# Kernel tuning notes

Measured on AMD Instinct MI355X. Metric: run time of the kernel, lower is better.

The kernel has to match this reference:

```python
import jax, jax.numpy as jnp
import numpy as np

B, N, K, C, CE, H = 2, 2048, 48, 128, 128, 128
IN = 2 * C + CE  # 384
AGG_SCALE = 30.0
LN_EPS = 1e-5


def setup_inputs() -> dict:
    key = jax.random.key(0)
    ks = jax.random.split(key, 12)
    inp = {
        "node_h": jax.random.normal(ks[0], (B, N, C), jnp.float32),
        "edge_h": jax.random.normal(ks[1], (B, N, K, CE), jnp.float32),
        "edge_index": jax.random.randint(ks[2], (B, N, K), 0, N, jnp.int64),
        # message MLP: Linear(IN,H) GELU Linear(H,H) GELU Linear(H,C)
        "W1": jax.random.normal(ks[3], (IN, H), jnp.float32) / np.sqrt(IN),
        "b1": jnp.zeros((H,), jnp.float32),
        "W2": jax.random.normal(ks[4], (H, H), jnp.float32) / np.sqrt(H),
        "b2": jnp.zeros((H,), jnp.float32),
        "W3": jax.random.normal(ks[5], (H, C), jnp.float32) / np.sqrt(H),
        "b3": jnp.zeros((C,), jnp.float32),
        "Wu": jax.random.normal(ks[6], (C, C), jnp.float32) / np.sqrt(C),
        "bu": jnp.zeros((C,), jnp.float32),
        "ln_g": jnp.ones((C,), jnp.float32),
        "ln_b": jnp.zeros((C,), jnp.float32),
    }
    return inp


def _layer_norm(x, g, b):
    mu = jnp.mean(x, axis=-1, keepdims=True)
    var = jnp.var(x, axis=-1, keepdims=True)
    return (x - mu) * jax.lax.rsqrt(var + LN_EPS) * g + b


def _gelu(x):
    return jax.nn.gelu(x, approximate=False)  # torch nn.GELU default (erf)


def reference(node_h, edge_h, edge_index, W1, b1, W2, b2, W3, b3, Wu, bu, ln_g, ln_b):
    b, n, k = edge_index.shape
    c = node_h.shape[-1]
    # gather neighbor node features: (B,N,K,C)
    node_j = jnp.take_along_axis(
        node_h, edge_index.reshape(b, n * k)[..., None], axis=1
    ).reshape(b, n, k, c)
    node_i = jnp.broadcast_to(node_h[:, :, None, :], (b, n, k, c))
    edge_packed = jnp.concatenate([node_i, node_j, edge_h], axis=-1)  # (B,N,K,IN)
    # message MLP
    h = _gelu(edge_packed @ W1 + b1)
    h = _gelu(h @ W2 + b2)
    messages = (h @ W3 + b3).sum(axis=-2) / AGG_SCALE  # (B,N,C)
    # dropout is identity in eval mode
    updated_nodes = _layer_norm(node_h + messages, ln_g, ln_b)
    node_updates = updated_nodes @ Wu + bu
    out = _layer_norm(node_h + node_updates, ln_g, ln_b)
    return out
```

## Files before the change

### kernel.cpp

```cpp
#include <hip/hip_runtime.h>
#include <hip/hip_bf16.h>
#include <math.h>

#define Bn   2
#define Nn   2048
#define Kn   48
#define Cn   128
#define G2   16

typedef short bf16x8 __attribute__((ext_vector_type(8)));
typedef float f32x4  __attribute__((ext_vector_type(4)));

#if __has_builtin(__builtin_amdgcn_cvt_pk_bf16_f32)
#define HAS_PK 1
#endif

__device__ __forceinline__ short f2bf(float f) {
  union { float f; unsigned u; } v; v.f = f;
  unsigned r = v.u + 0x7fffu + ((v.u >> 16) & 1u);
  return (short)(r >> 16);
}

__device__ __forceinline__ unsigned pk2(float a, float b) {
#ifdef HAS_PK
  auto p = __builtin_amdgcn_cvt_pk_bf16_f32(a, b);
  return __builtin_bit_cast(unsigned, p);
#else
  return (unsigned)(unsigned short)f2bf(a) | ((unsigned)(unsigned short)f2bf(b) << 16);
#endif
}

__device__ __forceinline__ float gelu_f(float x) {
  float z = x * (-2.3021991f - 0.10294200f * x * x);
  float e = __builtin_amdgcn_exp2f(z);
  return x * __builtin_amdgcn_rcpf(1.0f + e);
}

__global__ void pack_weights(const float* __restrict__ W1,
                             const float* __restrict__ W2,
                             const float* __restrict__ W3,
                             const float* __restrict__ Wu,
                             short* __restrict__ ws) {
  int tid = blockIdx.x * blockDim.x + threadIdx.x;
  if (tid >= 192 * 64) return;
  int lane = tid & 63;
  int tile = tid >> 6;
  const float* W; short* dst;
  if (tile < 32)       { W = W1;         dst = ws; }
  else if (tile < 96)  { W = W1 + 16384; dst = ws + 16384; tile -= 32; }
  else if (tile < 128) { W = W2;         dst = ws + 49152; tile -= 96; }
  else if (tile < 160) { W = W3;         dst = ws + 65536; tile -= 128; }
  else                 { W = Wu;         dst = ws + 81920; tile -= 160; }
  int kt = tile >> 3, nt = tile & 7;
  int n  = nt * 16 + (lane & 15);
  int k0 = kt * 32 + (lane >> 4) * 8;
  union { short s[8]; bf16x8 v; } u8;
#pragma unroll
  for (int j = 0; j < 8; j++) u8.s[j] = f2bf(W[(k0 + j) * 128 + n]);
  *reinterpret_cast<bf16x8*>(dst + (tile << 9) + lane * 8) = u8.v;
}

__global__ __launch_bounds__(256, 6)
void node_update_kernel(const float* __restrict__ node_h,
                        const float* __restrict__ edge_h,
                        const int*   __restrict__ edge_index,
                        const short* __restrict__ wpack,
                        const float* __restrict__ b1,
                        const float* __restrict__ b2,
                        float* __restrict__ hs_out) {
  __shared__ __align__(16) char smem[25024];
  short* Xs    = (short*)smem;
  short* H1s   = (short*)(smem + 12288);
  short* nhb   = (short*)(smem + 24576);
  int*   idx_s = (int*)  (smem + 24832);

  const int tid  = threadIdx.x;
  const int blk  = blockIdx.x;
  const int bb   = blk >> 11;
  const int lane = tid & 63;
  const int wave = tid >> 6;
  const int lr   = lane & 15;
  const int lq   = lane >> 4;

  const short* W1i = wpack;
  const short* W1e = wpack + 16384;
  const short* W2p = wpack + 49152;

  if (tid < 128) {
    nhb[tid] = f2bf(node_h[(size_t)blk * Cn + tid]);
  } else if (tid < 176) {
    idx_s[tid - 128] = edge_index[blk * Kn + (tid - 128)];
  }
  __syncthreads();

  {
    const int w  = tid & 31;
    const int rr = tid >> 5;
#pragma unroll
    for (int k = 0; k < 6; k++) {
      int r = rr + k * 8;
      const float* src = (w < 16)
          ? node_h + (size_t)(bb * Nn + idx_s[r]) * Cn + w * 8
          : edge_h + ((size_t)blk * Kn + r) * Cn + (w - 16) * 8;
      float4 v0 = *reinterpret_cast<const float4*>(src);
      float4 v1 = *reinterpret_cast<const float4*>(src + 4);
      uint4 p;
      p.x = pk2(v0.x, v0.y); p.y = pk2(v0.z, v0.w);
      p.z = pk2(v1.x, v1.y); p.w = pk2(v1.z, v1.w);
      *reinterpret_cast<uint4*>(&Xs[r * 256 + ((w ^ (r & 7)) << 3)]) = p;
    }
  }

  f32x4 accY[2] = {};
#pragma unroll
  for (int kt = 0; kt < 4; kt++) {
    bf16x8 av = {};
    if (lr == 0) av = *reinterpret_cast<const bf16x8*>(&nhb[kt * 32 + lq * 8]);
    bf16x8 bv0 = *reinterpret_cast<const bf16x8*>(W1i + ((kt * 8 + wave * 2 + 0) << 9) + lane * 8);
    bf16x8 bv1 = *reinterpret_cast<const bf16x8*>(W1i + ((kt * 8 + wave * 2 + 1) << 9) + lane * 8);
    accY[0] = __builtin_amdgcn_mfma_f32_16x16x32_bf16(av, bv0, accY[0], 0, 0, 0);
    accY[1] = __builtin_amdgcn_mfma_f32_16x16x32_bf16(av, bv1, accY[1], 0, 0, 0);
  }
  __syncthreads();

  f32x4 acc[3][2] = {};
#pragma unroll
  for (int kt = 0; kt < 8; kt++) {
    bf16x8 bf0 = *reinterpret_cast<const bf16x8*>(W1e + ((kt * 8 + wave * 2 + 0) << 9) + lane * 8);
    bf16x8 bf1 = *reinterpret_cast<const bf16x8*>(W1e + ((kt * 8 + wave * 2 + 1) << 9) + lane * 8);
    int sw = (((kt * 4 + lq) ^ (lr & 7)) << 3);
    bf16x8 a0 = *reinterpret_cast<const bf16x8*>(&Xs[(0  + lr) * 256 + sw]);
    bf16x8 a1 = *reinterpret_cast<const bf16x8*>(&Xs[(16 + lr) * 256 + sw]);
    bf16x8 a2 = *reinterpret_cast<const bf16x8*>(&Xs[(32 + lr) * 256 + sw]);
    acc[0][0] = __builtin_amdgcn_mfma_f32_16x16x32_bf16(a0, bf0, acc[0][0], 0, 0, 0);
    acc[0][1] = __builtin_amdgcn_mfma_f32_16x16x32_bf16(a0, bf1, acc[0][1], 0, 0, 0);
    acc[1][0] = __builtin_amdgcn_mfma_f32_16x16x32_bf16(a1, bf0, acc[1][0], 0, 0, 0);
    acc[1][1] = __builtin_amdgcn_mfma_f32_16x16x32_bf16(a1, bf1, acc[1][1], 0, 0, 0);
    acc[2][0] = __builtin_amdgcn_mfma_f32_16x16x32_bf16(a2, bf0, acc[2][0], 0, 0, 0);
    acc[2][1] = __builtin_amdgcn_mfma_f32_16x16x32_bf16(a2, bf1, acc[2][1], 0, 0, 0);
  }
  __syncthreads();

#pragma unroll
  for (int j = 0; j < 2; j++) {
    int col = (wave * 2 + j) * 16 + lr;
    float yi = __shfl(accY[j][0], lr) + b1[col];
    int g = col >> 3, cl = col & 7;
#pragma unroll
    for (int mt = 0; mt < 3; mt++) {
      int r0 = mt * 16 + lq * 4;
      float g0 = gelu_f(acc[mt][j][0] + yi);
      float g1 = gelu_f(acc[mt][j][1] + yi);
      float g2 = gelu_f(acc[mt][j][2] + yi);
      float g3 = gelu_f(acc[mt][j][3] + yi);
      unsigned p01 = pk2(g0, g1), p23 = pk2(g2, g3);
      H1s[(r0 + 0) * 128 + ((g ^ ((r0 + 0) & 7)) << 3) + cl] = (short)(p01 & 0xffff);
      H1s[(r0 + 1) * 128 + ((g ^ ((r0 + 1) & 7)) << 3) + cl] = (short)(p01 >> 16);
      H1s[(r0 + 2) * 128 + ((g ^ ((r0 + 2) & 7)) << 3) + cl] = (short)(p23 & 0xffff);
      H1s[(r0 + 3) * 128 + ((g ^ ((r0 + 3) & 7)) << 3) + cl] = (short)(p23 >> 16);
    }
  }
  __syncthreads();

  f32x4 acc2[3][2] = {};
#pragma unroll
  for (int kt = 0; kt < 4; kt++) {
    bf16x8 bf0 = *reinterpret_cast<const bf16x8*>(W2p + ((kt * 8 + wave * 2 + 0) << 9) + lane * 8);
    bf16x8 bf1 = *reinterpret_cast<const bf16x8*>(W2p + ((kt * 8 + wave * 2 + 1) << 9) + lane * 8);
    int sw = (((kt * 4 + lq) ^ (lr & 7)) << 3);
    bf16x8 a0 = *reinterpret_cast<const bf16x8*>(&H1s[(0  + lr) * 128 + sw]);
    bf16x8 a1 = *reinterpret_cast<const bf16x8*>(&H1s[(16 + lr) * 128 + sw]);
    bf16x8 a2 = *reinterpret_cast<const bf16x8*>(&H1s[(32 + lr) * 128 + sw]);
    acc2[0][0] = __builtin_amdgcn_mfma_f32_16x16x32_bf16(a0, bf0, acc2[0][0], 0, 0, 0);
    acc2[0][1] = __builtin_amdgcn_mfma_f32_16x16x32_bf16(a0, bf1, acc2[0][1], 0, 0, 0);
    acc2[1][0] = __builtin_amdgcn_mfma_f32_16x16x32_bf16(a1, bf0, acc2[1][0], 0, 0, 0);
    acc2[1][1] = __builtin_amdgcn_mfma_f32_16x16x32_bf16(a1, bf1, acc2[1][1], 0, 0, 0);
    acc2[2][0] = __builtin_amdgcn_mfma_f32_16x16x32_bf16(a2, bf0, acc2[2][0], 0, 0, 0);
    acc2[2][1] = __builtin_amdgcn_mfma_f32_16x16x32_bf16(a2, bf1, acc2[2][1], 0, 0, 0);
  }
#pragma unroll
  for (int j = 0; j < 2; j++) {
    int col = (wave * 2 + j) * 16 + lr;
    float bias = b2[col];
    float s = 0.f;
#pragma unroll
    for (int mt = 0; mt < 3; mt++)
#pragma unroll
      for (int r = 0; r < 4; r++) s += gelu_f(acc2[mt][j][r] + bias);
    s += __shfl_xor(s, 16);
    s += __shfl_xor(s, 32);
    if (lq == 0) hs_out[(size_t)blk * Cn + col] = s;
  }
}

__global__ __launch_bounds__(256, 4)
void tail_kernel(const float* __restrict__ node_h,
                 const short* __restrict__ wpack,
                 const float* __restrict__ b3,
                 const float* __restrict__ bu,
                 const float* __restrict__ ln_g,
                 const float* __restrict__ ln_b,
                 float* __restrict__ out) {
  __shared__ __align__(16) char sm2[24832];
  short* hsB = (short*)sm2;
  float* nhr = (float*)(sm2 + 4096);
  float* xs  = (float*)(sm2 + 12288);
  short* usB = (short*)(sm2 + 20736);

  const int tid  = threadIdx.x;
  const int lane = tid & 63;
  const int wave = tid >> 6;
  const int lr   = lane & 15;
  const int lq   = lane >> 4;
  const int n0   = blockIdx.x * G2;

  const short* W3p = wpack + 65536;
  const short* Wup = wpack + 81920;

  {
    int row = tid >> 4, seg = tid & 15;
    const float* p = node_h + (size_t)(n0 + row) * Cn + seg * 8;
    float4 a0 = *reinterpret_cast<const float4*>(p);
    float4 a1 = *reinterpret_cast<const float4*>(p + 4);
    *reinterpret_cast<float4*>(&nhr[row * 128 + seg * 8])     = a0;
    *reinterpret_cast<float4*>(&nhr[row * 128 + seg * 8 + 4]) = a1;
    const float* q = out + (size_t)(n0 + row) * Cn + seg * 8;
    float4 c0 = *reinterpret_cast<const float4*>(q);
    float4 c1 = *reinterpret_cast<const float4*>(q + 4);
    uint4 pk;
    pk.x = pk2(c0.x, c0.y); pk.y = pk2(c0.z, c0.w);
    pk.z = pk2(c1.x, c1.y); pk.w = pk2(c1.z, c1.w);
    *reinterpret_cast<uint4*>(&hsB[row * 128 + ((seg ^ (row & 7)) << 3)]) = pk;
  }
  __syncthreads();

  f32x4 am[2] = {};
#pragma unroll
  for (int kt = 0; kt < 4; kt++) {
    bf16x8 av = *reinterpret_cast<const bf16x8*>(&hsB[lr * 128 + (((kt * 4 + lq) ^ (lr & 7)) << 3)]);
    bf16x8 bv0 = *reinterpret_cast<const bf16x8*>(W3p + ((kt * 8 + wave * 2 + 0) << 9) + lane * 8);
    bf16x8 bv1 = *reinterpret_cast<const bf16x8*>(W3p + ((kt * 8 + wave * 2 + 1) << 9) + lane * 8);
    am[0] = __builtin_amdgcn_mfma_f32_16x16x32_bf16(av, bv0, am[0], 0, 0, 0);
    am[1] = __builtin_amdgcn_mfma_f32_16x16x32_bf16(av, bv1, am[1], 0, 0, 0);
  }
#pragma unroll
  for (int j = 0; j < 2; j++) {
    int col = (wave * 2 + j) * 16 + lr;
    float bb = 48.0f * b3[col];
#pragma unroll
    for (int r = 0; r < 4; r++) {
      int row = lq * 4 + r;
      xs[row * 132 + col] = nhr[row * 128 + col] + (am[j][r] + bb) * (1.0f / 30.0f);
    }
  }
  __syncthreads();

  const float lg1 = ln_g[lane],      lb1v = ln_b[lane];
  const float lg2 = ln_g[lane + 64], lb2v = ln_b[lane + 64];
#pragma unroll
  for (int s = 0; s < 4; s++) {
    int row = wave * 4 + s;
    float v1 = xs[row * 132 + lane];
    float v2 = xs[row * 132 + lane + 64];
    float s1 = v1 + v2, s2 = v1 * v1 + v2 * v2;
#pragma unroll
    for (int off = 32; off >= 1; off >>= 1) {
      s1 += __shfl_xor(s1, off);
      s2 += __shfl_xor(s2, off);
    }
    float mu = s1 * (1.f / 128.f);
    float var = s2 * (1.f / 128.f) - mu * mu;
    float rstd = rsqrtf(var + 1e-5f);
    unsigned u12 = pk2((v1 - mu) * rstd * lg1 + lb1v,
                       (v2 - mu) * rstd * lg2 + lb2v);
    int sw = (row & 7);
    usB[row * 128 + (((lane >> 3) ^ sw) << 3) + (lane & 7)]       = (short)(u12 & 0xffff);
    usB[row * 128 + ((((lane >> 3) + 8) ^ sw) << 3) + (lane & 7)] = (short)(u12 >> 16);
  }
  __syncthreads();

  f32x4 au[2] = {};
#pragma unroll
  for (int kt = 0; kt < 4; kt++) {
    bf16x8 av = *reinterpret_cast<const bf16x8*>(&usB[lr * 128 + (((kt * 4 + lq) ^ (lr & 7)) << 3)]);
    bf16x8 bv0 = *reinterpret_cast<const bf16x8*>(Wup + ((kt * 8 + wave * 2 + 0) << 9) + lane * 8);
    bf16x8 bv1 = *reinterpret_cast<const bf16x8*>(Wup + ((kt * 8 + wave * 2 + 1) << 9) + lane * 8);
    au[0] = __builtin_amdgcn_mfma_f32_16x16x32_bf16(av, bv0, au[0], 0, 0, 0);
    au[1] = __builtin_amdgcn_mfma_f32_16x16x32_bf16(av, bv1, au[1], 0, 0, 0);
  }
  __syncthreads();
#pragma unroll
  for (int j = 0; j < 2; j++) {
    int col = (wave * 2 + j) * 16 + lr;
    float bb = bu[col];
#pragma unroll
    for (int r = 0; r < 4; r++) {
      int row = lq * 4 + r;
      xs[row * 132 + col] = nhr[row * 128 + col] + au[j][r] + bb;
    }
  }
  __syncthreads();

#pragma unroll
  for (int s = 0; s < 4; s++) {
    int row = wave * 4 + s;
    float v1 = xs[row * 132 + lane];
    float v2 = xs[row * 132 + lane + 64];
    float s1 = v1 + v2, s2 = v1 * v1 + v2 * v2;
#pragma unroll
    for (int off = 32; off >= 1; off >>= 1) {
      s1 += __shfl_xor(s1, off);
      s2 += __shfl_xor(s2, off);
    }
    float mu = s1 * (1.f / 128.f);
    float var = s2 * (1.f / 128.f) - mu * mu;
    float rstd = rsqrtf(var + 1e-5f);
    out[(size_t)(n0 + row) * Cn + lane]      = (v1 - mu) * rstd * lg1 + lb1v;
    out[(size_t)(n0 + row) * Cn + lane + 64] = (v2 - mu) * rstd * lg2 + lb2v;
  }
}

extern "C" void kernel_launch(void* const* d_in, const int* in_sizes, int n_in,
                              void* d_out, int out_size, void* d_ws, size_t ws_size,
                              hipStream_t stream) {
  const float* node_h     = (const float*)d_in[0];
  const float* edge_h     = (const float*)d_in[1];
  const int*   edge_index = (const int*)  d_in[2];
  const float* W1 = (const float*)d_in[3];
  const float* b1 = (const float*)d_in[4];
  const float* W2 = (const float*)d_in[5];
  const float* b2 = (const float*)d_in[6];
  const float* W3 = (const float*)d_in[7];
  const float* b3 = (const float*)d_in[8];
  const float* Wu = (const float*)d_in[9];
  const float* bu = (const float*)d_in[10];
  const float* ln_g = (const float*)d_in[11];
  const float* ln_b = (const float*)d_in[12];
  float* out   = (float*)d_out;
  short* wpack = (short*)d_ws;

  pack_weights<<<48, 256, 0, stream>>>(W1, W2, W3, Wu, wpack);
  node_update_kernel<<<Bn * Nn, 256, 0, stream>>>(
      node_h, edge_h, edge_index, wpack, b1, b2, out);
  tail_kernel<<<(Bn * Nn) / G2, 256, 0, stream>>>(
      node_h, wpack, b3, bu, ln_g, ln_b, out);
}
```

Measured before the change: 204.5 us.

## Fuse tail W3/LayerNorm/Wu/LayerNorm stage into per-node message kernel

Removes the separate tail kernel and runs the W3 projection, both LayerNorms and the Wu projection at the end of the per-node kernel, one node per block. The aim is to drop a kernel launch and the global round-trip of the aggregated hidden sums. The cost is poor MFMA use: a single row is padded to 16 (only lr==0 lanes feed data), and the main kernel gains extra barriers and serial tail work per block.

```diff
diff --git a/kernel.cpp b/kernel.cpp
--- a/kernel.cpp
+++ b/kernel.cpp
@@ -6,7 +6,6 @@
 #define Nn   2048
 #define Kn   48
 #define Cn   128
-#define G2   16
 
 typedef short bf16x8 __attribute__((ext_vector_type(8)));
 typedef float f32x4  __attribute__((ext_vector_type(4)));
@@ -67,12 +66,19 @@
                         const short* __restrict__ wpack,
                         const float* __restrict__ b1,
                         const float* __restrict__ b2,
-                        float* __restrict__ hs_out) {
+                        const float* __restrict__ b3,
+                        const float* __restrict__ bu,
+                        const float* __restrict__ ln_g,
+                        const float* __restrict__ ln_b,
+                        float* __restrict__ out) {
   __shared__ __align__(16) char smem[25024];
   short* Xs    = (short*)smem;
   short* H1s   = (short*)(smem + 12288);
   short* nhb   = (short*)(smem + 24576);
   int*   idx_s = (int*)  (smem + 24832);
+  short* hsA   = (short*)smem;
+  float* xsA   = (float*)(smem + 512);
+  short* usA   = (short*)(smem + 1024);
 
   const int tid  = threadIdx.x;
   const int blk  = blockIdx.x;
@@ -85,6 +91,8 @@
   const short* W1i = wpack;
   const short* W1e = wpack + 16384;
   const short* W2p = wpack + 49152;
+  const short* W3p = wpack + 65536;
+  const short* Wup = wpack + 81920;
 
   if (tid < 128) {
     nhb[tid] = f2bf(node_h[(size_t)blk * Cn + tid]);
@@ -189,79 +197,32 @@
       for (int r = 0; r < 4; r++) s += gelu_f(acc2[mt][j][r] + bias);
     s += __shfl_xor(s, 16);
     s += __shfl_xor(s, 32);
-    if (lq == 0) hs_out[(size_t)blk * Cn + col] = s;
-  }
-}
-
-__global__ __launch_bounds__(256, 4)
-void tail_kernel(const float* __restrict__ node_h,
-                 const short* __restrict__ wpack,
-                 const float* __restrict__ b3,
-                 const float* __restrict__ bu,
-                 const float* __restrict__ ln_g,
-                 const float* __restrict__ ln_b,
-                 float* __restrict__ out) {
-  __shared__ __align__(16) char sm2[24832];
-  short* hsB = (short*)sm2;
-  float* nhr = (float*)(sm2 + 4096);
-  float* xs  = (float*)(sm2 + 12288);
-  short* usB = (short*)(sm2 + 20736);
-
-  const int tid  = threadIdx.x;
-  const int lane = tid & 63;
-  const int wave = tid >> 6;
-  const int lr   = lane & 15;
-  const int lq   = lane >> 4;
-  const int n0   = blockIdx.x * G2;
-
-  const short* W3p = wpack + 65536;
-  const short* Wup = wpack + 81920;
-
-  {
-    int row = tid >> 4, seg = tid & 15;
-    const float* p = node_h + (size_t)(n0 + row) * Cn + seg * 8;
-    float4 a0 = *reinterpret_cast<const float4*>(p);
-    float4 a1 = *reinterpret_cast<const float4*>(p + 4);
-    *reinterpret_cast<float4*>(&nhr[row * 128 + seg * 8])     = a0;
-    *reinterpret_cast<float4*>(&nhr[row * 128 + seg * 8 + 4]) = a1;
-    const float* q = out + (size_t)(n0 + row) * Cn + seg * 8;
-    float4 c0 = *reinterpret_cast<const float4*>(q);
-    float4 c1 = *reinterpret_cast<const float4*>(q + 4);
-    uint4 pk;
-    pk.x = pk2(c0.x, c0.y); pk.y = pk2(c0.z, c0.w);
-    pk.z = pk2(c1.x, c1.y); pk.w = pk2(c1.z, c1.w);
-    *reinterpret_cast<uint4*>(&hsB[row * 128 + ((seg ^ (row & 7)) << 3)]) = pk;
-  }
-  __syncthreads();
-
-  f32x4 am[2] = {};
-#pragma unroll
-  for (int kt = 0; kt < 4; kt++) {
-    bf16x8 av = *reinterpret_cast<const bf16x8*>(&hsB[lr * 128 + (((kt * 4 + lq) ^ (lr & 7)) << 3)]);
+    if (lq == 0) hsA[col] = f2bf(s);
+  }
+  __syncthreads();
+
+  f32x4 mv[2] = {};
+#pragma unroll
+  for (int kt = 0; kt < 4; kt++) {
+    bf16x8 av = {};
+    if (lr == 0) av = *reinterpret_cast<const bf16x8*>(&hsA[kt * 32 + lq * 8]);
     bf16x8 bv0 = *reinterpret_cast<const bf16x8*>(W3p + ((kt * 8 + wave * 2 + 0) << 9) + lane * 8);
     bf16x8 bv1 = *reinterpret_cast<const bf16x8*>(W3p + ((kt * 8 + wave * 2 + 1) << 9) + lane * 8);
-    am[0] = __builtin_amdgcn_mfma_f32_16x16x32_bf16(av, bv0, am[0], 0, 0, 0);
-    am[1] = __builtin_amdgcn_mfma_f32_16x16x32_bf16(av, bv1, am[1], 0, 0, 0);
-  }
-#pragma unroll
-  for (int j = 0; j < 2; j++) {
-    int col = (wave * 2 + j) * 16 + lr;
-    float bb = 48.0f * b3[col];
-#pragma unroll
-    for (int r = 0; r < 4; r++) {
-      int row = lq * 4 + r;
-      xs[row * 132 + col] = nhr[row * 128 + col] + (am[j][r] + bb) * (1.0f / 30.0f);
-    }
-  }
-  __syncthreads();
-
-  const float lg1 = ln_g[lane],      lb1v = ln_b[lane];
-  const float lg2 = ln_g[lane + 64], lb2v = ln_b[lane + 64];
-#pragma unroll
-  for (int s = 0; s < 4; s++) {
-    int row = wave * 4 + s;
-    float v1 = xs[row * 132 + lane];
-    float v2 = xs[row * 132 + lane + 64];
+    mv[0] = __builtin_amdgcn_mfma_f32_16x16x32_bf16(av, bv0, mv[0], 0, 0, 0);
+    mv[1] = __builtin_amdgcn_mfma_f32_16x16x32_bf16(av, bv1, mv[1], 0, 0, 0);
+  }
+  if (lq == 0) {
+#pragma unroll
+    for (int j = 0; j < 2; j++) {
+      int col = (wave * 2 + j) * 16 + lr;
+      xsA[col] = node_h[(size_t)blk * Cn + col]
+               + (mv[j][0] + 48.0f * b3[col]) * (1.0f / 30.0f);
+    }
+  }
+  __syncthreads();
+
+  if (wave == 0) {
+    float v1 = xsA[lane], v2 = xsA[lane + 64];
     float s1 = v1 + v2, s2 = v1 * v1 + v2 * v2;
 #pragma unroll
     for (int off = 32; off >= 1; off >>= 1) {
@@ -271,41 +232,34 @@
     float mu = s1 * (1.f / 128.f);
     float var = s2 * (1.f / 128.f) - mu * mu;
     float rstd = rsqrtf(var + 1e-5f);
-    unsigned u12 = pk2((v1 - mu) * rstd * lg1 + lb1v,
-                       (v2 - mu) * rstd * lg2 + lb2v);
-    int sw = (row & 7);
-    usB[row * 128 + (((lane >> 3) ^ sw) << 3) + (lane & 7)]       = (short)(u12 & 0xffff);
-    usB[row * 128 + ((((lane >> 3) + 8) ^ sw) << 3) + (lane & 7)] = (short)(u12 >> 16);
-  }
-  __syncthreads();
-
-  f32x4 au[2] = {};
-#pragma unroll
-  for (int kt = 0; kt < 4; kt++) {
-    bf16x8 av = *reinterpret_cast<const bf16x8*>(&usB[lr * 128 + (((kt * 4 + lq) ^ (lr & 7)) << 3)]);
+    unsigned u12 = pk2((v1 - mu) * rstd * ln_g[lane] + ln_b[lane],
+                       (v2 - mu) * rstd * ln_g[lane + 64] + ln_b[lane + 64]);
+    usA[lane]      = (short)(u12 & 0xffff);
+    usA[lane + 64] = (short)(u12 >> 16);
+  }
+  __syncthreads();
+
+  f32x4 uv[2] = {};
+#pragma unroll
+  for (int kt = 0; kt < 4; kt++) {
+    bf16x8 av = {};
+    if (lr == 0) av = *reinterpret_cast<const bf16x8*>(&usA[kt * 32 + lq * 8]);
     bf16x8 bv0 = *reinterpret_cast<const bf16x8*>(Wup + ((kt * 8 + wave * 2 + 0) << 9) + lane * 8);
     bf16x8 bv1 = *reinterpret_cast<const bf16x8*>(Wup + ((kt * 8 + wave * 2 + 1) << 9) + lane * 8);
-    au[0] = __builtin_amdgcn_mfma_f32_16x16x32_bf16(av, bv0, au[0], 0, 0, 0);
-    au[1] = __builtin_amdgcn_mfma_f32_16x16x32_bf16(av, bv1, au[1], 0, 0, 0);
-  }
-  __syncthreads();
-#pragma unroll
-  for (int j = 0; j < 2; j++) {
-    int col = (wave * 2 + j) * 16 + lr;
-    float bb = bu[col];
-#pragma unroll
-    for (int r = 0; r < 4; r++) {
-      int row = lq * 4 + r;
-      xs[row * 132 + col] = nhr[row * 128 + col] + au[j][r] + bb;
-    }
-  }
-  __syncthreads();
-
-#pragma unroll
-  for (int s = 0; s < 4; s++) {
-    int row = wave * 4 + s;
-    float v1 = xs[row * 132 + lane];
-    float v2 = xs[row * 132 + lane + 64];
+    uv[0] = __builtin_amdgcn_mfma_f32_16x16x32_bf16(av, bv0, uv[0], 0, 0, 0);
+    uv[1] = __builtin_amdgcn_mfma_f32_16x16x32_bf16(av, bv1, uv[1], 0, 0, 0);
+  }
+  if (lq == 0) {
+#pragma unroll
+    for (int j = 0; j < 2; j++) {
+      int col = (wave * 2 + j) * 16 + lr;
+      xsA[col] = node_h[(size_t)blk * Cn + col] + uv[j][0] + bu[col];
+    }
+  }
+  __syncthreads();
+
+  if (wave == 0) {
+    float v1 = xsA[lane], v2 = xsA[lane + 64];
     float s1 = v1 + v2, s2 = v1 * v1 + v2 * v2;
 #pragma unroll
     for (int off = 32; off >= 1; off >>= 1) {
@@ -315,8 +269,8 @@
     float mu = s1 * (1.f / 128.f);
     float var = s2 * (1.f / 128.f) - mu * mu;
     float rstd = rsqrtf(var + 1e-5f);
-    out[(size_t)(n0 + row) * Cn + lane]      = (v1 - mu) * rstd * lg1 + lb1v;
-    out[(size_t)(n0 + row) * Cn + lane + 64] = (v2 - mu) * rstd * lg2 + lb2v;
+    out[(size_t)blk * Cn + lane]      = (v1 - mu) * rstd * ln_g[lane] + ln_b[lane];
+    out[(size_t)blk * Cn + lane + 64] = (v2 - mu) * rstd * ln_g[lane + 64] + ln_b[lane + 64];
   }
 }
 
@@ -341,7 +295,5 @@
 
   pack_weights<<<48, 256, 0, stream>>>(W1, W2, W3, Wu, wpack);
   node_update_kernel<<<Bn * Nn, 256, 0, stream>>>(
-      node_h, edge_h, edge_index, wpack, b1, b2, out);
-  tail_kernel<<<(Bn * Nn) / G2, 256, 0, stream>>>(
-      node_h, wpack, b3, bu, ln_g, ln_b, out);
-}
+      node_h, edge_h, edge_index, wpack, b1, b2, b3, bu, ln_g, ln_b, out);
+}
```

New measurement: 220.1 us. +7.6%, slower.

## Process two nodes per block with eight waves each owning one output column tile

Applied to the files above, without the earlier changes.

The node update kernel now handles two nodes per 512-thread block, giving 96 edge rows per block. Each of the eight waves owns a single 16-column output tile and loops over six row tiles, so each wave loads half as many weight fragments per row. This is meant to cut the global weight fragment traffic per edge and halve the block count. The cost is doubled shared memory per block (about 50 KB) and a larger block size, which may limit how many blocks fit on a CU.

```diff
diff --git a/kernel.cpp b/kernel.cpp
--- a/kernel.cpp
+++ b/kernel.cpp
@@ -60,7 +60,7 @@
   *reinterpret_cast<bf16x8*>(dst + (tile << 9) + lane * 8) = u8.v;
 }
 
-__global__ __launch_bounds__(256, 6)
+__global__ __launch_bounds__(512, 6)
 void node_update_kernel(const float* __restrict__ node_h,
                         const float* __restrict__ edge_h,
                         const int*   __restrict__ edge_index,
@@ -68,15 +68,15 @@
                         const float* __restrict__ b1,
                         const float* __restrict__ b2,
                         float* __restrict__ hs_out) {
-  __shared__ __align__(16) char smem[25024];
+  __shared__ __align__(16) char smem[50048];
   short* Xs    = (short*)smem;
-  short* H1s   = (short*)(smem + 12288);
-  short* nhb   = (short*)(smem + 24576);
-  int*   idx_s = (int*)  (smem + 24832);
+  short* H1s   = (short*)(smem + 24576);
+  short* nhb   = (short*)(smem + 49152);
+  int*   idx_s = (int*)  (smem + 49664);
 
   const int tid  = threadIdx.x;
-  const int blk  = blockIdx.x;
-  const int bb   = blk >> 11;
+  const int n0   = blockIdx.x * 2;
+  const int bb   = n0 >> 11;
   const int lane = tid & 63;
   const int wave = tid >> 6;
   const int lr   = lane & 15;
@@ -86,10 +86,10 @@
   const short* W1e = wpack + 16384;
   const short* W2p = wpack + 49152;
 
-  if (tid < 128) {
-    nhb[tid] = f2bf(node_h[(size_t)blk * Cn + tid]);
-  } else if (tid < 176) {
-    idx_s[tid - 128] = edge_index[blk * Kn + (tid - 128)];
+  if (tid < 256) {
+    nhb[tid] = f2bf(node_h[(size_t)n0 * Cn + tid]);
+  } else if (tid < 352) {
+    idx_s[tid - 256] = edge_index[n0 * Kn + (tid - 256)];
   }
   __syncthreads();
 
@@ -98,10 +98,10 @@
     const int rr = tid >> 5;
 #pragma unroll
     for (int k = 0; k < 6; k++) {
-      int r = rr + k * 8;
+      int r = rr + k * 16;
       const float* src = (w < 16)
           ? node_h + (size_t)(bb * Nn + idx_s[r]) * Cn + w * 8
-          : edge_h + ((size_t)blk * Kn + r) * Cn + (w - 16) * 8;
+          : edge_h + ((size_t)n0 * Kn + r) * Cn + (w - 16) * 8;
       float4 v0 = *reinterpret_cast<const float4*>(src);
       float4 v1 = *reinterpret_cast<const float4*>(src + 4);
       uint4 p;
@@ -114,45 +114,43 @@
   f32x4 accY[2] = {};
 #pragma unroll
   for (int kt = 0; kt < 4; kt++) {
-    bf16x8 av = {};
-    if (lr == 0) av = *reinterpret_cast<const bf16x8*>(&nhb[kt * 32 + lq * 8]);
-    bf16x8 bv0 = *reinterpret_cast<const bf16x8*>(W1i + ((kt * 8 + wave * 2 + 0) << 9) + lane * 8);
-    bf16x8 bv1 = *reinterpret_cast<const bf16x8*>(W1i + ((kt * 8 + wave * 2 + 1) << 9) + lane * 8);
-    accY[0] = __builtin_amdgcn_mfma_f32_16x16x32_bf16(av, bv0, accY[0], 0, 0, 0);
-    accY[1] = __builtin_amdgcn_mfma_f32_16x16x32_bf16(av, bv1, accY[1], 0, 0, 0);
-  }
-  __syncthreads();
-
-  f32x4 acc[3][2] = {};
+    bf16x8 avA = {}, avB = {};
+    if (lr == 0) {
+      avA = *reinterpret_cast<const bf16x8*>(&nhb[kt * 32 + lq * 8]);
+      avB = *reinterpret_cast<const bf16x8*>(&nhb[128 + kt * 32 + lq * 8]);
+    }
+    bf16x8 bv = *reinterpret_cast<const bf16x8*>(W1i + ((kt * 8 + wave) << 9) + lane * 8);
+    accY[0] = __builtin_amdgcn_mfma_f32_16x16x32_bf16(avA, bv, accY[0], 0, 0, 0);
+    accY[1] = __builtin_amdgcn_mfma_f32_16x16x32_bf16(avB, bv, accY[1], 0, 0, 0);
+  }
+  __syncthreads();
+
+  f32x4 acc[6] = {};
 #pragma unroll
   for (int kt = 0; kt < 8; kt++) {
-    bf16x8 bf0 = *reinterpret_cast<const bf16x8*>(W1e + ((kt * 8 + wave * 2 + 0) << 9) + lane * 8);
-    bf16x8 bf1 = *reinterpret_cast<const bf16x8*>(W1e + ((kt * 8 + wave * 2 + 1) << 9) + lane * 8);
+    bf16x8 bf = *reinterpret_cast<const bf16x8*>(W1e + ((kt * 8 + wave) << 9) + lane * 8);
     int sw = (((kt * 4 + lq) ^ (lr & 7)) << 3);
-    bf16x8 a0 = *reinterpret_cast<const bf16x8*>(&Xs[(0  + lr) * 256 + sw]);
-    bf16x8 a1 = *reinterpret_cast<const bf16x8*>(&Xs[(16 + lr) * 256 + sw]);
-    bf16x8 a2 = *reinterpret_cast<const bf16x8*>(&Xs[(32 + lr) * 256 + sw]);
-    acc[0][0] = __builtin_amdgcn_mfma_f32_16x16x32_bf16(a0, bf0, acc[0][0], 0, 0, 0);
-    acc[0][1] = __builtin_amdgcn_mfma_f32_16x16x32_bf16(a0, bf1, acc[0][1], 0, 0, 0);
-    acc[1][0] = __builtin_amdgcn_mfma_f32_16x16x32_bf16(a1, bf0, acc[1][0], 0, 0, 0);
-    acc[1][1] = __builtin_amdgcn_mfma_f32_16x16x32_bf16(a1, bf1, acc[1][1], 0, 0, 0);
-    acc[2][0] = __builtin_amdgcn_mfma_f32_16x16x32_bf16(a2, bf0, acc[2][0], 0, 0, 0);
-    acc[2][1] = __builtin_amdgcn_mfma_f32_16x16x32_bf16(a2, bf1, acc[2][1], 0, 0, 0);
-  }
-  __syncthreads();
-
-#pragma unroll
-  for (int j = 0; j < 2; j++) {
-    int col = (wave * 2 + j) * 16 + lr;
-    float yi = __shfl(accY[j][0], lr) + b1[col];
+#pragma unroll
+    for (int m = 0; m < 6; m++) {
+      bf16x8 a = *reinterpret_cast<const bf16x8*>(&Xs[(m * 16 + lr) * 256 + sw]);
+      acc[m] = __builtin_amdgcn_mfma_f32_16x16x32_bf16(a, bf, acc[m], 0, 0, 0);
+    }
+  }
+  __syncthreads();
+
+  {
+    int col = wave * 16 + lr;
+    float yiA = __shfl(accY[0][0], lr) + b1[col];
+    float yiB = __shfl(accY[1][0], lr) + b1[col];
     int g = col >> 3, cl = col & 7;
 #pragma unroll
-    for (int mt = 0; mt < 3; mt++) {
+    for (int mt = 0; mt < 6; mt++) {
+      float yi = (mt < 3) ? yiA : yiB;
       int r0 = mt * 16 + lq * 4;
-      float g0 = gelu_f(acc[mt][j][0] + yi);
-      float g1 = gelu_f(acc[mt][j][1] + yi);
-      float g2 = gelu_f(acc[mt][j][2] + yi);
-      float g3 = gelu_f(acc[mt][j][3] + yi);
+      float g0 = gelu_f(acc[mt][0] + yi);
+      float g1 = gelu_f(acc[mt][1] + yi);
+      float g2 = gelu_f(acc[mt][2] + yi);
+      float g3 = gelu_f(acc[mt][3] + yi);
       unsigned p01 = pk2(g0, g1), p23 = pk2(g2, g3);
       H1s[(r0 + 0) * 128 + ((g ^ ((r0 + 0) & 7)) << 3) + cl] = (short)(p01 & 0xffff);
       H1s[(r0 + 1) * 128 + ((g ^ ((r0 + 1) & 7)) << 3) + cl] = (short)(p01 >> 16);
@@ -162,34 +160,36 @@
   }
   __syncthreads();
 
-  f32x4 acc2[3][2] = {};
+  f32x4 acc2[6] = {};
 #pragma unroll
   for (int kt = 0; kt < 4; kt++) {
-    bf16x8 bf0 = *reinterpret_cast<const bf16x8*>(W2p + ((kt * 8 + wave * 2 + 0) << 9) + lane * 8);
-    bf16x8 bf1 = *reinterpret_cast<const bf16x8*>(W2p + ((kt * 8 + wave * 2 + 1) << 9) + lane * 8);
+    bf16x8 bf = *reinterpret_cast<const bf16x8*>(W2p + ((kt * 8 + wave) << 9) + lane * 8);
     int sw = (((kt * 4 + lq) ^ (lr & 7)) << 3);
-    bf16x8 a0 = *reinterpret_cast<const bf16x8*>(&H1s[(0  + lr) * 128 + sw]);
-    bf16x8 a1 = *reinterpret_cast<const bf16x8*>(&H1s[(16 + lr) * 128 + sw]);
-    bf16x8 a2 = *reinterpret_cast<const bf16x8*>(&H1s[(32 + lr) * 128 + sw]);
-    acc2[0][0] = __builtin_amdgcn_mfma_f32_16x16x32_bf16(a0, bf0, acc2[0][0], 0, 0, 0);
-    acc2[0][1] = __builtin_amdgcn_mfma_f32_16x16x32_bf16(a0, bf1, acc2[0][1], 0, 0, 0);
-    acc2[1][0] = __builtin_amdgcn_mfma_f32_16x16x32_bf16(a1, bf0, acc2[1][0], 0, 0, 0);
-    acc2[1][1] = __builtin_amdgcn_mfma_f32_16x16x32_bf16(a1, bf1, acc2[1][1], 0, 0, 0);
-    acc2[2][0] = __builtin_amdgcn_mfma_f32_16x16x32_bf16(a2, bf0, acc2[2][0], 0, 0, 0);
-    acc2[2][1] = __builtin_amdgcn_mfma_f32_16x16x32_bf16(a2, bf1, acc2[2][1], 0, 0, 0);
-  }
-#pragma unroll
-  for (int j = 0; j < 2; j++) {
-    int col = (wave * 2 + j) * 16 + lr;
+#pragma unroll
+    for (int m = 0; m < 6; m++) {
+      bf16x8 a = *reinterpret_cast<const bf16x8*>(&H1s[(m * 16 + lr) * 128 + sw]);
+      acc2[m] = __builtin_amdgcn_mfma_f32_16x16x32_bf16(a, bf, acc2[m], 0, 0, 0);
+    }
+  }
+  {
+    int col = wave * 16 + lr;
     float bias = b2[col];
-    float s = 0.f;
+    float sA = 0.f, sB = 0.f;
 #pragma unroll
     for (int mt = 0; mt < 3; mt++)
 #pragma unroll
-      for (int r = 0; r < 4; r++) s += gelu_f(acc2[mt][j][r] + bias);
-    s += __shfl_xor(s, 16);
-    s += __shfl_xor(s, 32);
-    if (lq == 0) hs_out[(size_t)blk * Cn + col] = s;
+      for (int r = 0; r < 4; r++) {
+        sA += gelu_f(acc2[mt][r] + bias);
+        sB += gelu_f(acc2[mt + 3][r] + bias);
+      }
+    sA += __shfl_xor(sA, 16);
+    sA += __shfl_xor(sA, 32);
+    sB += __shfl_xor(sB, 16);
+    sB += __shfl_xor(sB, 32);
+    if (lq == 0) {
+      hs_out[(size_t)n0 * Cn + col]       = sA;
+      hs_out[(size_t)(n0 + 1) * Cn + col] = sB;
+    }
   }
 }
 
@@ -340,7 +340,7 @@
   short* wpack = (short*)d_ws;
 
   pack_weights<<<48, 256, 0, stream>>>(W1, W2, W3, Wu, wpack);
-  node_update_kernel<<<Bn * Nn, 256, 0, stream>>>(
+  node_update_kernel<<<(Bn * Nn) / 2, 512, 0, stream>>>(
       node_h, edge_h, edge_index, wpack, b1, b2, out);
   tail_kernel<<<(Bn * Nn) / G2, 256, 0, stream>>>(
       node_h, wpack, b3, bu, ln_g, ln_b, out);
```

New measurement: 206.7 us. About the same (+1.0%).
